# Optimization experiments

Hardware: AMD Instinct MI355X
Metric: run time of the kernel (lower is better)

## Reference

```python
import jax, jax.numpy as jnp
import numpy as np

B, SEQ = 64, 128
WV, PV = 50000, 50
WE, PE = 100, 25
HID = 400
DA, DR, NR = 500, 100, 46

_PARAMS = [
    ('word_emb', (WV, WE)), ('pos_emb', (PV, PE)),
    ('wi0f', (4*HID, WE+PE)), ('wh0f', (4*HID, HID)), ('b0f', (4*HID,)),
    ('wi0b', (4*HID, WE+PE)), ('wh0b', (4*HID, HID)), ('b0b', (4*HID,)),
    ('wi1f', (4*HID, 2*HID)), ('wh1f', (4*HID, HID)), ('b1f', (4*HID,)),
    ('wi1b', (4*HID, 2*HID)), ('wh1b', (4*HID, HID)), ('b1b', (4*HID,)),
    ('wi2f', (4*HID, 2*HID)), ('wh2f', (4*HID, HID)), ('b2f', (4*HID,)),
    ('wi2b', (4*HID, 2*HID)), ('wh2b', (4*HID, HID)), ('b2b', (4*HID,)),
    ('Wad', (2*HID, DA)), ('bad', (DA,)), ('Wah', (2*HID, DA)), ('bah', (DA,)),
    ('Wrd', (2*HID, DR)), ('brd', (DR,)), ('Wrh', (2*HID, DR)), ('brh', (DR,)),
    ('W_arc', (DA, DA)), ('b_arc', (DA,)),
    ('U_rel', (DR, NR, DR)), ('W_rel', (DR, NR)), ('b_rel', (NR,)),
]


def _run_dir(x, wi, wh, b, reverse):
    # x: (B, T, in). PyTorch LSTM gate order: i, f, g, o.
    pre = jnp.swapaxes(x, 0, 1) @ wi.T + b  # (T, B, 4H) input projection hoisted out of scan
    h0 = jnp.zeros((x.shape[0], wh.shape[1]), x.dtype)

    def step(carry, p):
        hp, cp = carry
        z = p + hp @ wh.T
        i, f, g, o = jnp.split(z, 4, axis=-1)
        c = jax.nn.sigmoid(f) * cp + jax.nn.sigmoid(i) * jnp.tanh(g)
        hn = jax.nn.sigmoid(o) * jnp.tanh(c)
        return (hn, c), hn

    _, ys = jax.lax.scan(step, (h0, h0), pre, reverse=reverse)
    return jnp.swapaxes(ys, 0, 1)  # (B, T, H)


def _bilstm(x, fwd, bwd):
    return jnp.concatenate([_run_dir(x, *fwd, reverse=False),
                            _run_dir(x, *bwd, reverse=True)], axis=-1)


def _forward(p, words, pos):
    # Embedding lookup + concat (dropout = identity in eval math)
    x = jnp.concatenate([p['word_emb'][words], p['pos_emb'][pos]], axis=-1)  # (B,SEQ,125)
    h = _bilstm(x, (p['wi0f'], p['wh0f'], p['b0f']), (p['wi0b'], p['wh0b'], p['b0b']))
    h = _bilstm(h, (p['wi1f'], p['wh1f'], p['b1f']), (p['wi1b'], p['wh1b'], p['b1b']))
    h = _bilstm(h, (p['wi2f'], p['wh2f'], p['b2f']), (p['wi2b'], p['wh2b'], p['b2b']))  # (B,SEQ,800)
    H_ah = jax.nn.relu(h @ p['Wah'] + p['bah'])
    H_ad = jax.nn.relu(h @ p['Wad'] + p['bad'])
    H_rh = jax.nn.relu(h @ p['Wrh'] + p['brh'])
    H_rd = jax.nn.relu(h @ p['Wrd'] + p['brd'])
    # Biaffine arc scores: S[b,i,j] = H_ad[b,i] W_arc H_ah[b,j] + b_arc . H_ah[b,j]
    S = jnp.einsum('bid,de,bje->bij', H_ad, p['W_arc'], H_ah) + (H_ah @ p['b_arc'])[:, None, :]
    head_preds = jnp.argmax(S, axis=2)  # (B, SEQ)
    # Original double python loop builds one_hot and bmm's it; that is exactly a row gather:
    H_rh_sel = jnp.take_along_axis(H_rh, head_preds[..., None], axis=1)  # (B,SEQ,DR)
    inter = jnp.einsum('bid,drk,bik->bir', H_rh_sel, p['U_rel'], H_rd)   # (B,SEQ,NR)
    sums = (H_rh_sel + H_rd) @ p['W_rel'] + p['b_rel']
    return S, inter + sums, head_preds


def setup_inputs() -> dict:
    key = jax.random.key(0)
    ks = jax.random.split(key, len(_PARAMS) + 2)
    out = {name: jax.random.normal(k, shape, jnp.float32) * 0.1
           for k, (name, shape) in zip(ks[:-2], _PARAMS)}
    out['words'] = jax.random.randint(ks[-2], (B, SEQ), 0, WV)
    out['pos'] = jax.random.randint(ks[-1], (B, SEQ), 0, PV)
    return out


def reference(words, pos, word_emb, pos_emb, wi0f, wh0f, b0f, wi0b, wh0b, b0b,
              wi1f, wh1f, b1f, wi1b, wh1b, b1b, wi2f, wh2f, b2f, wi2b, wh2b, b2b,
              Wad, bad, Wah, bah, Wrd, brd, Wrh, brh, W_arc, b_arc, U_rel, W_rel, b_rel):
    names = [n for n, _ in _PARAMS]
    vals = [word_emb, pos_emb, wi0f, wh0f, b0f, wi0b, wh0b, b0b,
            wi1f, wh1f, b1f, wi1b, wh1b, b1b, wi2f, wh2f, b2f, wi2b, wh2b, b2b,
            Wad, bad, Wah, bah, Wrd, brd, Wrh, brh, W_arc, b_arc, U_rel, W_rel, b_rel]
    return _forward(dict(zip(names, vals)), words, pos)
```

## Files before the change

### kernel.cpp

```cpp
#include <hip/hip_runtime.h>


#define TT 128
#define HID 400
#define G4 1600
#define NTOK 8192
#define NWD 100
#define CH 16

__global__ void embed_k(const int* __restrict__ words, const int* __restrict__ pos,
                        const float* __restrict__ wemb, const float* __restrict__ pemb,
                        float* __restrict__ x0) {
    int m = blockIdx.x;
    int t = m >> 6, b = m & 63;
    int tid = threadIdx.x;
    if (tid < 100) {
        x0[(size_t)m * 125 + tid] = wemb[(size_t)words[b * TT + t] * 100 + tid];
    } else if (tid < 125) {
        x0[(size_t)m * 125 + tid] = pemb[(size_t)pos[b * TT + t] * 25 + (tid - 100)];
    }
}

template <bool L0>
__global__ __launch_bounds__(256) void pre_k(
    const float* __restrict__ x0, const double* __restrict__ hF, const double* __restrict__ hB,
    const float* __restrict__ wiF, const float* __restrict__ wiB,
    const float* __restrict__ bF, const float* __restrict__ bB,
    double* __restrict__ prF, double* __restrict__ prB, int m0F, int m0B) {
    const int dir = blockIdx.z;
    const float* wi = dir ? wiB : wiF;
    const float* bias = dir ? bB : bF;
    double* pr = dir ? prB : prF;
    const int m0 = dir ? m0B : m0F;
    const int KP = L0 ? 128 : 800;

    __shared__ double As[16][66];
    __shared__ double Bs[16][66];

    const int tid = threadIdx.x;
    const int tm = tid >> 4, tn = tid & 15;
    const int bn = blockIdx.x * 64;
    const int y = blockIdx.y;
    const int tt = (m0 >> 6) + y;
    const int lane = tid & 63, kq = tid >> 6;

    double acc[4][4];
#pragma unroll
    for (int i = 0; i < 4; i++)
#pragma unroll
        for (int j = 0; j < 4; j++) acc[i][j] = 0.0;

    for (int k0 = 0; k0 < KP; k0 += 16) {
        if (L0) {
#pragma unroll
            for (int u = 0; u < 4; u++) {
                int k = k0 + kq * 4 + u;
                As[kq * 4 + u][lane] = (k < 125) ? (double)wi[(size_t)(bn + lane) * 125 + k] : 0.0;
            }
        } else {
            const float4 wv = *(const float4*)&wi[(size_t)(bn + lane) * 800 + k0 + kq * 4];
            As[kq * 4 + 0][lane] = (double)wv.x;
            As[kq * 4 + 1][lane] = (double)wv.y;
            As[kq * 4 + 2][lane] = (double)wv.z;
            As[kq * 4 + 3][lane] = (double)wv.w;
        }
        if (L0) {
#pragma unroll
            for (int u = 0; u < 4; u++) {
                int k = k0 + kq * 4 + u;
                Bs[kq * 4 + u][lane] = (k < 125) ? (double)x0[((size_t)tt * 64 + lane) * 125 + k] : 0.0;
            }
        } else {
            int kbase = k0 + kq * 4;
            const double* src = (kbase < 400) ? hF : hB;
            int kb = (kbase < 400) ? kbase : kbase - 400;
            const double* p = src + (size_t)tt * 25600 + (size_t)kb * 64 + lane;
#pragma unroll
            for (int u = 0; u < 4; u++) Bs[kq * 4 + u][lane] = p[(size_t)u * 64];
        }
        __syncthreads();
#pragma unroll
        for (int kk = 0; kk < 16; kk++) {
            double a[4], b[4];
#pragma unroll
            for (int i = 0; i < 4; i++) a[i] = As[kk][tm * 4 + i];
#pragma unroll
            for (int j = 0; j < 4; j++) b[j] = Bs[kk][tn * 4 + j];
#pragma unroll
            for (int i = 0; i < 4; i++)
#pragma unroll
                for (int j = 0; j < 4; j++) acc[i][j] = fma(a[i], b[j], acc[i][j]);
        }
        __syncthreads();
    }
#pragma unroll
    for (int i = 0; i < 4; i++) {
        int n = bn + tm * 4 + i;
        double bv = (double)bias[n];
#pragma unroll
        for (int j = 0; j < 4; j++)
            pr[((size_t)y * G4 + n) * 64 + (tn * 4 + j)] = acc[i][j] + bv;
    }
}

template <bool SPLITA, bool RELU, typename TC>
__global__ __launch_bounds__(256) void heads_k(
    const double* __restrict__ A, const double* __restrict__ AF, const double* __restrict__ AB,
    const float* __restrict__ Bm, const float* __restrict__ bias, TC* __restrict__ C,
    int N, int K, int ldb, int ldc, int OM) {
    __shared__ double As[16][66];
    __shared__ double Bs[16][66];
    const int tid = threadIdx.x;
    const int tm = tid >> 4, tn = tid & 15;
    const int bn = blockIdx.x * 64;
    const int bm = blockIdx.y * 64;
    const int lane = tid & 63, kq = tid >> 6;

    double acc[4][4];
#pragma unroll
    for (int i = 0; i < 4; i++)
#pragma unroll
        for (int j = 0; j < 4; j++) acc[i][j] = 0.0;

    const int KP = (K + 15) & ~15;
    for (int k0 = 0; k0 < KP; k0 += 16) {
        if (SPLITA) {
            int kbase = k0 + kq * 4;
            const double* src = (kbase < 400) ? AF : AB;
            int kb = (kbase < 400) ? kbase : kbase - 400;
            const double* p = src + (size_t)(bm >> 6) * 25600 + (size_t)kb * 64 + lane;
#pragma unroll
            for (int u = 0; u < 4; u++) As[kq * 4 + u][lane] = p[(size_t)u * 64];
        } else {
#pragma unroll
            for (int u = 0; u < 4; u++) {
                int k = k0 + kq * 4 + u;
                As[kq * 4 + u][lane] = (k < K) ? A[(size_t)(bm + lane) * K + k] : 0.0;
            }
        }
        {
            bool nok = (bn + lane) < N;
#pragma unroll
            for (int u = 0; u < 4; u++) {
                int k = k0 + kq * 4 + u;
                Bs[kq * 4 + u][lane] = (nok && k < K) ? (double)Bm[(size_t)k * ldb + bn + lane] : 0.0;
            }
        }
        __syncthreads();
#pragma unroll
        for (int kk = 0; kk < 16; kk++) {
            double a[4], b[4];
#pragma unroll
            for (int i = 0; i < 4; i++) a[i] = As[kk][tm * 4 + i];
#pragma unroll
            for (int j = 0; j < 4; j++) b[j] = Bs[kk][tn * 4 + j];
#pragma unroll
            for (int i = 0; i < 4; i++)
#pragma unroll
                for (int j = 0; j < 4; j++) acc[i][j] = fma(a[i], b[j], acc[i][j]);
        }
        __syncthreads();
    }
#pragma unroll
    for (int i = 0; i < 4; i++) {
        int row = bm + tm * 4 + i;
        size_t orow = (OM == 0) ? (size_t)row
                                : ((size_t)(row & 63) * TT + (row >> 6));
#pragma unroll
        for (int j = 0; j < 4; j++) {
            int n = bn + tn * 4 + j;
            if (n >= N) continue;
            double v = acc[i][j] + (bias ? (double)bias[n] : 0.0);
            if (RELU) v = fmax(v, 0.0);
            C[orow * ldc + n] = (TC)v;
        }
    }
}

__global__ __launch_bounds__(512) void lstm_k(
    const double* __restrict__ preF, const double* __restrict__ preB,
    const float* __restrict__ whF, const float* __restrict__ whB,
    double* __restrict__ hsF, double* __restrict__ hsB,
    double* __restrict__ csF, double* __restrict__ csB,
    int* __restrict__ flagsF, int* __restrict__ flagsB, int ci) {
    const int wg = blockIdx.x;
    const int dir = wg / NWD;
    const int wgd = wg % NWD;
    const double* pre = dir ? preB : preF;
    const float* wh = dir ? whB : whF;
    double* hs = dir ? hsB : hsF;
    double* cs = dir ? csB : csF;
    int* flags = dir ? flagsB : flagsF;
    const int tid = threadIdx.x;
    const int b = tid & 63;
    const int w = tid >> 6;
    const int tlb = dir ? (TT - CH - ci * CH) : ci * CH;

    __shared__ double whl[4][HID][4];
    __shared__ double pl[8][4][4][64];
    for (int idx = tid; idx < 4 * HID * 4; idx += 512) {
        int g = idx & 3; int k = (idx >> 2) % HID; int jx = idx / (4 * HID);
        whl[jx][k][g] = (double)wh[((size_t)g * HID + wgd * 4 + jx) * HID + k];
    }
    __syncthreads();

    const int jown = wgd * 4 + (w & 3);
    double c = 0.0;
    if (w < 4) c = (ci == 0) ? 0.0 : cs[(size_t)jown * 64 + b];

    for (int s = 0; s < CH; ++s) {
        const int sg = ci * CH + s;
        const int t = dir ? (TT - 1 - sg) : sg;
        double z0[4];
        if (w < 4) {
            const double* pp = pre + (size_t)(t - tlb) * (G4 * 64) + b;
#pragma unroll
            for (int g = 0; g < 4; g++) z0[g] = pp[(size_t)(g * HID + jown) * 64];
        }
        if (sg > 0) {
            if (w == 0) {
                bool need2 = b < (NWD - 64);
                for (;;) {
                    int f1 = __hip_atomic_load(&flags[b], __ATOMIC_RELAXED, __HIP_MEMORY_SCOPE_AGENT);
                    int f2 = need2 ? __hip_atomic_load(&flags[64 + b], __ATOMIC_RELAXED, __HIP_MEMORY_SCOPE_AGENT)
                                   : 0x7fffffff;
                    if (__all(f1 >= sg && f2 >= sg)) break;
                    __builtin_amdgcn_s_sleep(1);
                }
                __builtin_amdgcn_fence(__ATOMIC_ACQUIRE, "agent");
            }
            __syncthreads();
        }
        double part[4][4];
#pragma unroll
        for (int j = 0; j < 4; j++)
#pragma unroll
            for (int g = 0; g < 4; g++) part[j][g] = 0.0;
        if (sg > 0) {
            const int tp = dir ? (t + 1) : (t - 1);
            const double* hp = hs + (size_t)tp * (HID * 64) + b;
#pragma unroll 5
            for (int k = w * 50; k < w * 50 + 50; ++k) {
                double hv = hp[(size_t)k * 64];
#pragma unroll
                for (int j = 0; j < 4; j++)
#pragma unroll
                    for (int g = 0; g < 4; g++)
                        part[j][g] = fma(hv, whl[j][k][g], part[j][g]);
            }
        }
#pragma unroll
        for (int j = 0; j < 4; j++)
#pragma unroll
            for (int g = 0; g < 4; g++) pl[w][j][g][b] = part[j][g];
        __syncthreads();
        if (w < 4) {
            double z[4];
#pragma unroll
            for (int g = 0; g < 4; g++) {
                double acc = z0[g];
#pragma unroll
                for (int q = 0; q < 8; q++) acc += pl[q][w][g][b];
                z[g] = acc;
            }
            double si = 1.0 / (1.0 + exp(-z[0]));
            double sf = 1.0 / (1.0 + exp(-z[1]));
            double tg = tanh(z[2]);
            double so = 1.0 / (1.0 + exp(-z[3]));
            c = sf * c + si * tg;
            double h = so * tanh(c);
            __hip_atomic_store(&hs[(size_t)t * (HID * 64) + (size_t)jown * 64 + b], h,
                               __ATOMIC_RELAXED, __HIP_MEMORY_SCOPE_AGENT);
        }
        __syncthreads();
        if (tid == 0)
            __hip_atomic_store(&flags[wgd], sg + 1, __ATOMIC_RELEASE, __HIP_MEMORY_SCOPE_AGENT);
    }
    if (w < 4) cs[(size_t)jown * 64 + b] = c;
}

__global__ void bh_k(const double* __restrict__ Hah, const float* __restrict__ barc,
                     double* __restrict__ bh) {
    int row = blockIdx.x * 4 + (threadIdx.x >> 6);
    int lane = threadIdx.x & 63;
    const double* r = Hah + (size_t)row * 500;
    double s = 0.0;
    for (int e = lane; e < 500; e += 64) s = fma(r[e], (double)barc[e], s);
    for (int off = 32; off; off >>= 1) s += __shfl_down(s, off, 64);
    if (lane == 0) bh[row] = s;
}

__global__ __launch_bounds__(256) void s_k(const double* __restrict__ HadW,
                                           const double* __restrict__ Hah,
                                           const double* __restrict__ bh,
                                           double* __restrict__ S64,
                                           float* __restrict__ Sf) {
    int b = blockIdx.z;
    int i = blockIdx.y * 16 + threadIdx.y;
    int j = blockIdx.x * 16 + threadIdx.x;
    const double* ra = HadW + ((size_t)b * TT + i) * 500;
    const double* rb = Hah + ((size_t)b * TT + j) * 500;
    double s = 0.0;
#pragma unroll 4
    for (int e = 0; e < 500; ++e) s = fma(ra[e], rb[e], s);
    double v = s + bh[b * TT + j];
    size_t o = ((size_t)b * TT + i) * TT + j;
    S64[o] = v;
    Sf[o] = (float)v;
}

__global__ void argmax_k(const double* __restrict__ S64, int* __restrict__ headi,
                         float* __restrict__ headf) {
    int row = blockIdx.x * 4 + (threadIdx.x >> 6);
    int lane = threadIdx.x & 63;
    const double* r = S64 + (size_t)row * TT;
    double v0 = r[lane], v1 = r[lane + 64];
    double m = fmax(v0, v1);
    for (int off = 32; off; off >>= 1) m = fmax(m, __shfl_down(m, off, 64));
    m = __shfl(m, 0, 64);
    double tau = 1e-4 + 3e-6 * fabs(m);
    int c = 999;
    if (v1 >= m - tau) c = lane + 64;
    if (v0 >= m - tau) c = lane;
    for (int off = 32; off; off >>= 1) {
        int oc = __shfl_down(c, off, 64);
        c = min(c, oc);
    }
    if (lane == 0) { headi[row] = c; headf[row] = (float)c; }
}

__global__ __launch_bounds__(320) void rel_k(
    const float* __restrict__ Hrh, const float* __restrict__ Hrd,
    const int* __restrict__ headi, const float* __restrict__ U,
    const float* __restrict__ Wrel, const float* __restrict__ brel,
    float* __restrict__ out) {
    __shared__ float sel[32][105];
    __shared__ float rd[32][105];
    __shared__ float red[32][12];
    int tid = threadIdx.x;
    int blk = blockIdx.x;
    for (int idx = tid; idx < 32 * 100; idx += 320) {
        int tt2 = idx / 100, d = idx % 100;
        int tok = blk * 32 + tt2;
        int b = tok >> 7;
        int hp = headi[tok] & 127;
        sel[tt2][d] = Hrh[((size_t)(b << 7) + hp) * 100 + d];
        rd[tt2][d] = Hrd[(size_t)tok * 100 + d];
    }
    __syncthreads();
    int tt2 = tid & 31;
    int dg = tid >> 5;
    int tok = blk * 32 + tt2;
    int r0 = blockIdx.y * 6;
    int r1 = min(46, r0 + 6);
    for (int r = r0; r < r1; ++r) {
        float acc = 0.f;
#pragma unroll
        for (int dd = 0; dd < 10; dd += 2) {
            int d = dg * 10 + dd;
            const float4* uA = (const float4*)(U + ((size_t)d * 46 + r) * 100);
            const float4* uB = (const float4*)(U + ((size_t)(d + 1) * 46 + r) * 100);
            float a0 = 0.f, a1 = 0.f, a2 = 0.f, a3 = 0.f;
            float b0 = 0.f, b1 = 0.f, b2 = 0.f, b3 = 0.f;
#pragma unroll
            for (int q = 0; q < 25; ++q) {
                float4 ua = uA[q], ub = uB[q];
                float r0v = rd[tt2][4 * q + 0], r1v = rd[tt2][4 * q + 1];
                float r2v = rd[tt2][4 * q + 2], r3v = rd[tt2][4 * q + 3];
                a0 = fmaf(ua.x, r0v, a0); a1 = fmaf(ua.y, r1v, a1);
                a2 = fmaf(ua.z, r2v, a2); a3 = fmaf(ua.w, r3v, a3);
                b0 = fmaf(ub.x, r0v, b0); b1 = fmaf(ub.y, r1v, b1);
                b2 = fmaf(ub.z, r2v, b2); b3 = fmaf(ub.w, r3v, b3);
            }
            acc = fmaf(sel[tt2][d], (a0 + a1) + (a2 + a3), acc);
            acc = fmaf(sel[tt2][d + 1], (b0 + b1) + (b2 + b3), acc);
        }
        if (dg == 0) {
            float sdot = 0.f;
#pragma unroll 4
            for (int k = 0; k < 100; ++k)
                sdot = fmaf(sel[tt2][k] + rd[tt2][k], Wrel[k * 46 + r], sdot);
            acc += sdot + brel[r];
        }
        red[tt2][dg] = acc;
        __syncthreads();
        if (dg == 0) {
            float tot = 0.f;
#pragma unroll
            for (int q = 0; q < 10; ++q) tot += red[tt2][q];
            out[(size_t)tok * 46 + r] = tot;
        }
        __syncthreads();
    }
}

extern "C" void kernel_launch(void* const* d_in, const int* in_sizes, int n_in,
                              void* d_out, int out_size, void* d_ws, size_t ws_size,
                              hipStream_t stream) {
    const float* wemb = (const float*)d_in[0];
    const float* pemb = (const float*)d_in[1];
    const float* wi[3][2] = {{(const float*)d_in[2], (const float*)d_in[5]},
                             {(const float*)d_in[8], (const float*)d_in[11]},
                             {(const float*)d_in[14], (const float*)d_in[17]}};
    const float* wh[3][2] = {{(const float*)d_in[3], (const float*)d_in[6]},
                             {(const float*)d_in[9], (const float*)d_in[12]},
                             {(const float*)d_in[15], (const float*)d_in[18]}};
    const float* bia[3][2] = {{(const float*)d_in[4], (const float*)d_in[7]},
                              {(const float*)d_in[10], (const float*)d_in[13]},
                              {(const float*)d_in[16], (const float*)d_in[19]}};
    const float* Wad = (const float*)d_in[20]; const float* bad = (const float*)d_in[21];
    const float* Wah = (const float*)d_in[22]; const float* bah = (const float*)d_in[23];
    const float* Wrd = (const float*)d_in[24]; const float* brd = (const float*)d_in[25];
    const float* Wrh = (const float*)d_in[26]; const float* brh = (const float*)d_in[27];
    const float* Warc = (const float*)d_in[28]; const float* barc = (const float*)d_in[29];
    const float* U = (const float*)d_in[30];
    const float* Wrel = (const float*)d_in[31]; const float* brel = (const float*)d_in[32];
    const int* words = (const int*)d_in[33];
    const int* pos = (const int*)d_in[34];

    char* ws = (char*)d_ws;
    double* hsA  = (double*)(ws + 0);
    double* hsB  = (double*)(ws + 52428800);
    float*  x0   = (float*)(ws + 52428800);
    double* preF = (double*)(ws + 104857600);
    double* preB = (double*)(ws + 117964800);
    double* Hah64  = (double*)(ws + 52428800);
    double* Had64  = (double*)(ws + 85196800);
    float*  Hrh    = (float*)(ws + 117964800);
    float*  Hrd    = (float*)(ws + 121241600);
    double* S64    = (double*)(ws + 124518400);
    double* bh64   = (double*)(ws + 132907008);
    int*    headi  = (int*)(ws + 132972544);
    double* HadW64 = (double*)(ws + 0);
    double* csF  = (double*)d_out;
    double* csB  = (double*)((char*)d_out + 204800);
    int*    flags = (int*)((char*)d_out + 409600);

    float* Sf = (float*)d_out;
    float* rel = Sf + 1048576;
    float* headf = Sf + 1425408;

    hipMemsetAsync(flags, 0, 768 * sizeof(int), stream);
    embed_k<<<NTOK, 128, 0, stream>>>(words, pos, wemb, pemb, x0);

    const size_t HALF = 3276800;
    dim3 gPre(25, CH, 2);
    for (int l = 0; l < 3; ++l) {
        double* ho = (l == 1) ? hsB : hsA;
        const double* hiF = (l == 0) ? nullptr : ((l == 1) ? hsA : hsB);
        const double* hiB = hiF ? hiF + HALF : nullptr;
        for (int ci = 0; ci < 8; ++ci) {
            int m0F = ci * CH * 64;
            int m0B = (TT - CH - ci * CH) * 64;
            if (l == 0)
                pre_k<true><<<gPre, 256, 0, stream>>>(x0, nullptr, nullptr,
                    wi[0][0], wi[0][1], bia[0][0], bia[0][1], preF, preB, m0F, m0B);
            else
                pre_k<false><<<gPre, 256, 0, stream>>>(nullptr, hiF, hiB,
                    wi[l][0], wi[l][1], bia[l][0], bia[l][1], preF, preB, m0F, m0B);
            lstm_k<<<2 * NWD, 512, 0, stream>>>(preF, preB, wh[l][0], wh[l][1],
                ho, ho + HALF, csF, csB,
                flags + (l * 2 + 0) * 128, flags + (l * 2 + 1) * 128, ci);
        }
    }
    const double* fF = hsA; const double* fB = hsA + HALF;
    heads_k<true, true, double><<<dim3(8, 128), 256, 0, stream>>>(
        nullptr, fF, fB, Wah, bah, Hah64, 500, 800, 500, 500, 1);
    heads_k<true, true, double><<<dim3(8, 128), 256, 0, stream>>>(
        nullptr, fF, fB, Wad, bad, Had64, 500, 800, 500, 500, 0);
    heads_k<true, true, float><<<dim3(2, 128), 256, 0, stream>>>(
        nullptr, fF, fB, Wrh, brh, Hrh, 100, 800, 100, 100, 1);
    heads_k<true, true, float><<<dim3(2, 128), 256, 0, stream>>>(
        nullptr, fF, fB, Wrd, brd, Hrd, 100, 800, 100, 100, 1);
    heads_k<false, false, double><<<dim3(8, 128), 256, 0, stream>>>(
        Had64, nullptr, nullptr, Warc, nullptr, HadW64, 500, 500, 500, 500, 1);

    bh_k<<<NTOK / 4, 256, 0, stream>>>(Hah64, barc, bh64);
    s_k<<<dim3(8, 8, 64), dim3(16, 16), 0, stream>>>(HadW64, Hah64, bh64, S64, Sf);
    argmax_k<<<NTOK / 4, 256, 0, stream>>>(S64, headi, headf);
    rel_k<<<dim3(NTOK / 32, 8), 320, 0, stream>>>(Hrh, Hrd, headi, U, Wrel, brel, rel);
}
```

Baseline: 10.63 ms.

## Fuse LSTM recurrence with next-chunk input projection in one double-buffered kernel

Merges the per-chunk input-projection GEMM and the LSTM recurrence into a single kernel. The first 200 blocks run the recurrence for chunk ci while the remaining blocks compute the projection for chunk ci+1 into a second, double-buffered pre-activation buffer. Chunk size is halved to 8 steps and there are 16 chunks per layer. The LSTM block also shrinks from 512 threads with a cross-wave partial-sum reduction to 256 threads, each wave owning one hidden unit and doing the full k loop. The GEMM thread-to-element mapping is changed to a strided layout, and the S dot product gets four independent accumulators. This hides projection time behind the serial recurrence, at the cost of more kernel launches and longer per-thread recurrence loops.

```diff
diff --git a/kernel.cpp b/kernel.cpp
--- a/kernel.cpp
+++ b/kernel.cpp
@@ -6,7 +6,8 @@
 #define G4 1600
 #define NTOK 8192
 #define NWD 100
-#define CH 16
+#define CH 8
+#define NCH 16
 
 __global__ void embed_k(const int* __restrict__ words, const int* __restrict__ pos,
                         const float* __restrict__ wemb, const float* __restrict__ pemb,
@@ -22,84 +23,158 @@
 }
 
 template <bool L0>
-__global__ __launch_bounds__(256) void pre_k(
+__global__ __launch_bounds__(256) void fused_k(
     const float* __restrict__ x0, const double* __restrict__ hF, const double* __restrict__ hB,
     const float* __restrict__ wiF, const float* __restrict__ wiB,
     const float* __restrict__ bF, const float* __restrict__ bB,
-    double* __restrict__ prF, double* __restrict__ prB, int m0F, int m0B) {
-    const int dir = blockIdx.z;
-    const float* wi = dir ? wiB : wiF;
-    const float* bias = dir ? bB : bF;
-    double* pr = dir ? prB : prF;
-    const int m0 = dir ? m0B : m0F;
-    const int KP = L0 ? 128 : 800;
-
-    __shared__ double As[16][66];
-    __shared__ double Bs[16][66];
-
+    double* __restrict__ preW, const double* __restrict__ preR,
+    const float* __restrict__ whF, const float* __restrict__ whB,
+    double* __restrict__ hsF, double* __restrict__ hsB,
+    double* __restrict__ csF, double* __restrict__ csB,
+    int* __restrict__ flagsF, int* __restrict__ flagsB,
+    int ci, int nLstm) {
+    __shared__ __align__(16) char smraw[51200];
     const int tid = threadIdx.x;
-    const int tm = tid >> 4, tn = tid & 15;
-    const int bn = blockIdx.x * 64;
-    const int y = blockIdx.y;
-    const int tt = (m0 >> 6) + y;
-    const int lane = tid & 63, kq = tid >> 6;
-
-    double acc[4][4];
-#pragma unroll
-    for (int i = 0; i < 4; i++)
-#pragma unroll
-        for (int j = 0; j < 4; j++) acc[i][j] = 0.0;
-
-    for (int k0 = 0; k0 < KP; k0 += 16) {
-        if (L0) {
-#pragma unroll
-            for (int u = 0; u < 4; u++) {
-                int k = k0 + kq * 4 + u;
-                As[kq * 4 + u][lane] = (k < 125) ? (double)wi[(size_t)(bn + lane) * 125 + k] : 0.0;
-            }
-        } else {
-            const float4 wv = *(const float4*)&wi[(size_t)(bn + lane) * 800 + k0 + kq * 4];
-            As[kq * 4 + 0][lane] = (double)wv.x;
-            As[kq * 4 + 1][lane] = (double)wv.y;
-            As[kq * 4 + 2][lane] = (double)wv.z;
-            As[kq * 4 + 3][lane] = (double)wv.w;
-        }
-        if (L0) {
-#pragma unroll
-            for (int u = 0; u < 4; u++) {
-                int k = k0 + kq * 4 + u;
-                Bs[kq * 4 + u][lane] = (k < 125) ? (double)x0[((size_t)tt * 64 + lane) * 125 + k] : 0.0;
-            }
-        } else {
-            int kbase = k0 + kq * 4;
-            const double* src = (kbase < 400) ? hF : hB;
-            int kb = (kbase < 400) ? kbase : kbase - 400;
-            const double* p = src + (size_t)tt * 25600 + (size_t)kb * 64 + lane;
-#pragma unroll
-            for (int u = 0; u < 4; u++) Bs[kq * 4 + u][lane] = p[(size_t)u * 64];
+
+    if ((int)blockIdx.x < nLstm) {
+        double (*whl)[HID][4] = (double(*)[HID][4])smraw;
+        const int wg = blockIdx.x;
+        const int dir = wg / NWD;
+        const int wgd = wg % NWD;
+        const double* pre = preR + (size_t)dir * 819200;
+        const float* wh = dir ? whB : whF;
+        double* hs = dir ? hsB : hsF;
+        double* cs = dir ? csB : csF;
+        int* flags = dir ? flagsB : flagsF;
+        const int b = tid & 63;
+        const int w = tid >> 6;
+        const int tlb = dir ? (TT - CH - ci * CH) : ci * CH;
+
+        for (int idx = tid; idx < 4 * HID * 4; idx += 256) {
+            int g = idx & 3; int k = (idx >> 2) % HID; int jx = idx / (4 * HID);
+            whl[jx][k][g] = (double)wh[((size_t)g * HID + wgd * 4 + jx) * HID + k];
         }
         __syncthreads();
-#pragma unroll
-        for (int kk = 0; kk < 16; kk++) {
-            double a[4], b[4];
-#pragma unroll
-            for (int i = 0; i < 4; i++) a[i] = As[kk][tm * 4 + i];
-#pragma unroll
-            for (int j = 0; j < 4; j++) b[j] = Bs[kk][tn * 4 + j];
-#pragma unroll
-            for (int i = 0; i < 4; i++)
-#pragma unroll
-                for (int j = 0; j < 4; j++) acc[i][j] = fma(a[i], b[j], acc[i][j]);
-        }
-        __syncthreads();
-    }
-#pragma unroll
-    for (int i = 0; i < 4; i++) {
-        int n = bn + tm * 4 + i;
-        double bv = (double)bias[n];
-#pragma unroll
-        for (int j = 0; j < 4; j++)
-            pr[((size_t)y * G4 + n) * 64 + (tn * 4 + j)] = acc[i][j] + bv;
+
+        const int jown = wgd * 4 + w;
+        double c = (ci == 0) ? 0.0 : cs[(size_t)jown * 64 + b];
+
+        for (int s = 0; s < CH; ++s) {
+            const int sg = ci * CH + s;
+            const int t = dir ? (TT - 1 - sg) : sg;
+            double z[4];
+            {
+                const double* pp = pre + (size_t)(t - tlb) * (G4 * 64) + b;
+#pragma unroll
+                for (int g = 0; g < 4; g++) z[g] = pp[(size_t)(g * HID + jown) * 64];
+            }
+            if (sg > 0) {
+                if (w == 0) {
+                    bool need2 = b < (NWD - 64);
+                    for (;;) {
+                        int f1 = __hip_atomic_load(&flags[b], __ATOMIC_RELAXED, __HIP_MEMORY_SCOPE_AGENT);
+                        int f2 = need2 ? __hip_atomic_load(&flags[64 + b], __ATOMIC_RELAXED, __HIP_MEMORY_SCOPE_AGENT)
+                                       : 0x7fffffff;
+                        if (__all(f1 >= sg && f2 >= sg)) break;
+                        __builtin_amdgcn_s_sleep(1);
+                    }
+                    __builtin_amdgcn_fence(__ATOMIC_ACQUIRE, "agent");
+                }
+                __syncthreads();
+                const int tp = dir ? (t + 1) : (t - 1);
+                const double* hp = hs + (size_t)tp * (HID * 64) + b;
+#pragma unroll 4
+                for (int k = 0; k < HID; ++k) {
+                    double hv = hp[(size_t)k * 64];
+                    const double* w4 = &whl[w][k][0];
+                    z[0] = fma(hv, w4[0], z[0]);
+                    z[1] = fma(hv, w4[1], z[1]);
+                    z[2] = fma(hv, w4[2], z[2]);
+                    z[3] = fma(hv, w4[3], z[3]);
+                }
+            }
+            double si = 1.0 / (1.0 + exp(-z[0]));
+            double sf = 1.0 / (1.0 + exp(-z[1]));
+            double tg = tanh(z[2]);
+            double so = 1.0 / (1.0 + exp(-z[3]));
+            c = sf * c + si * tg;
+            double h = so * tanh(c);
+            __hip_atomic_store(&hs[(size_t)t * (HID * 64) + (size_t)jown * 64 + b], h,
+                               __ATOMIC_RELAXED, __HIP_MEMORY_SCOPE_AGENT);
+            __syncthreads();
+            if (tid == 0)
+                __hip_atomic_store(&flags[wgd], sg + 1, __ATOMIC_RELEASE, __HIP_MEMORY_SCOPE_AGENT);
+        }
+        cs[(size_t)jown * 64 + b] = c;
+    } else {
+        const int cn = ci + 1;
+        if (cn >= NCH) return;
+        double (*As)[66] = (double(*)[66])smraw;
+        double (*Bs)[66] = (double(*)[66])(smraw + 8448);
+        int tile = blockIdx.x - nLstm;
+        int nt = tile % 25;
+        int rest = tile / 25;
+        int y = rest & 7;
+        int dirp = rest >> 3;
+        const float* wi = dirp ? wiB : wiF;
+        const float* bias = dirp ? bB : bF;
+        double* pr = preW + (size_t)dirp * 819200;
+        const int tt = dirp ? (TT - CH - cn * CH) + y : cn * CH + y;
+        const int bn = nt * 64;
+        const int tm = tid >> 4, tn = tid & 15;
+        const int lane = tid & 63, kq = tid >> 6;
+
+        double acc[4][4];
+#pragma unroll
+        for (int i = 0; i < 4; i++)
+#pragma unroll
+            for (int j = 0; j < 4; j++) acc[i][j] = 0.0;
+
+        const int KP = L0 ? 128 : 800;
+        for (int k0 = 0; k0 < KP; k0 += 16) {
+            if (L0) {
+#pragma unroll
+                for (int u = 0; u < 4; u++) {
+                    int k = k0 + kq * 4 + u;
+                    As[kq * 4 + u][lane] = (k < 125) ? (double)wi[(size_t)(bn + lane) * 125 + k] : 0.0;
+                    Bs[kq * 4 + u][lane] = (k < 125) ? (double)x0[((size_t)tt * 64 + lane) * 125 + k] : 0.0;
+                }
+            } else {
+                const float4 wv = *(const float4*)&wi[(size_t)(bn + lane) * 800 + k0 + kq * 4];
+                As[kq * 4 + 0][lane] = (double)wv.x;
+                As[kq * 4 + 1][lane] = (double)wv.y;
+                As[kq * 4 + 2][lane] = (double)wv.z;
+                As[kq * 4 + 3][lane] = (double)wv.w;
+                int kbase = k0 + kq * 4;
+                const double* src = (kbase < 400) ? hF : hB;
+                int kb = (kbase < 400) ? kbase : kbase - 400;
+                const double* p = src + (size_t)tt * 25600 + (size_t)kb * 64 + lane;
+#pragma unroll
+                for (int u = 0; u < 4; u++) Bs[kq * 4 + u][lane] = p[(size_t)u * 64];
+            }
+            __syncthreads();
+#pragma unroll
+            for (int kk = 0; kk < 16; kk++) {
+                double a[4], bv[4];
+#pragma unroll
+                for (int i = 0; i < 4; i++) a[i] = As[kk][i * 16 + tm];
+#pragma unroll
+                for (int j = 0; j < 4; j++) bv[j] = Bs[kk][j * 16 + tn];
+#pragma unroll
+                for (int i = 0; i < 4; i++)
+#pragma unroll
+                    for (int j = 0; j < 4; j++) acc[i][j] = fma(a[i], bv[j], acc[i][j]);
+            }
+            __syncthreads();
+        }
+#pragma unroll
+        for (int i = 0; i < 4; i++) {
+            int n = bn + i * 16 + tm;
+            double bv = (double)bias[n];
+#pragma unroll
+            for (int j = 0; j < 4; j++)
+                pr[((size_t)y * G4 + n) * 64 + (j * 16 + tn)] = acc[i][j] + bv;
+        }
     }
 }
 
@@ -149,134 +224,32 @@
         __syncthreads();
 #pragma unroll
         for (int kk = 0; kk < 16; kk++) {
-            double a[4], b[4];
-#pragma unroll
-            for (int i = 0; i < 4; i++) a[i] = As[kk][tm * 4 + i];
-#pragma unroll
-            for (int j = 0; j < 4; j++) b[j] = Bs[kk][tn * 4 + j];
+            double a[4], bv[4];
+#pragma unroll
+            for (int i = 0; i < 4; i++) a[i] = As[kk][i * 16 + tm];
+#pragma unroll
+            for (int j = 0; j < 4; j++) bv[j] = Bs[kk][j * 16 + tn];
 #pragma unroll
             for (int i = 0; i < 4; i++)
 #pragma unroll
-                for (int j = 0; j < 4; j++) acc[i][j] = fma(a[i], b[j], acc[i][j]);
+                for (int j = 0; j < 4; j++) acc[i][j] = fma(a[i], bv[j], acc[i][j]);
         }
         __syncthreads();
     }
 #pragma unroll
     for (int i = 0; i < 4; i++) {
-        int row = bm + tm * 4 + i;
+        int row = bm + i * 16 + tm;
         size_t orow = (OM == 0) ? (size_t)row
                                 : ((size_t)(row & 63) * TT + (row >> 6));
 #pragma unroll
         for (int j = 0; j < 4; j++) {
-            int n = bn + tn * 4 + j;
+            int n = bn + j * 16 + tn;
             if (n >= N) continue;
             double v = acc[i][j] + (bias ? (double)bias[n] : 0.0);
             if (RELU) v = fmax(v, 0.0);
             C[orow * ldc + n] = (TC)v;
         }
     }
-}
-
-__global__ __launch_bounds__(512) void lstm_k(
-    const double* __restrict__ preF, const double* __restrict__ preB,
-    const float* __restrict__ whF, const float* __restrict__ whB,
-    double* __restrict__ hsF, double* __restrict__ hsB,
-    double* __restrict__ csF, double* __restrict__ csB,
-    int* __restrict__ flagsF, int* __restrict__ flagsB, int ci) {
-    const int wg = blockIdx.x;
-    const int dir = wg / NWD;
-    const int wgd = wg % NWD;
-    const double* pre = dir ? preB : preF;
-    const float* wh = dir ? whB : whF;
-    double* hs = dir ? hsB : hsF;
-    double* cs = dir ? csB : csF;
-    int* flags = dir ? flagsB : flagsF;
-    const int tid = threadIdx.x;
-    const int b = tid & 63;
-    const int w = tid >> 6;
-    const int tlb = dir ? (TT - CH - ci * CH) : ci * CH;
-
-    __shared__ double whl[4][HID][4];
-    __shared__ double pl[8][4][4][64];
-    for (int idx = tid; idx < 4 * HID * 4; idx += 512) {
-        int g = idx & 3; int k = (idx >> 2) % HID; int jx = idx / (4 * HID);
-        whl[jx][k][g] = (double)wh[((size_t)g * HID + wgd * 4 + jx) * HID + k];
-    }
-    __syncthreads();
-
-    const int jown = wgd * 4 + (w & 3);
-    double c = 0.0;
-    if (w < 4) c = (ci == 0) ? 0.0 : cs[(size_t)jown * 64 + b];
-
-    for (int s = 0; s < CH; ++s) {
-        const int sg = ci * CH + s;
-        const int t = dir ? (TT - 1 - sg) : sg;
-        double z0[4];
-        if (w < 4) {
-            const double* pp = pre + (size_t)(t - tlb) * (G4 * 64) + b;
-#pragma unroll
-            for (int g = 0; g < 4; g++) z0[g] = pp[(size_t)(g * HID + jown) * 64];
-        }
-        if (sg > 0) {
-            if (w == 0) {
-                bool need2 = b < (NWD - 64);
-                for (;;) {
-                    int f1 = __hip_atomic_load(&flags[b], __ATOMIC_RELAXED, __HIP_MEMORY_SCOPE_AGENT);
-                    int f2 = need2 ? __hip_atomic_load(&flags[64 + b], __ATOMIC_RELAXED, __HIP_MEMORY_SCOPE_AGENT)
-                                   : 0x7fffffff;
-                    if (__all(f1 >= sg && f2 >= sg)) break;
-                    __builtin_amdgcn_s_sleep(1);
-                }
-                __builtin_amdgcn_fence(__ATOMIC_ACQUIRE, "agent");
-            }
-            __syncthreads();
-        }
-        double part[4][4];
-#pragma unroll
-        for (int j = 0; j < 4; j++)
-#pragma unroll
-            for (int g = 0; g < 4; g++) part[j][g] = 0.0;
-        if (sg > 0) {
-            const int tp = dir ? (t + 1) : (t - 1);
-            const double* hp = hs + (size_t)tp * (HID * 64) + b;
-#pragma unroll 5
-            for (int k = w * 50; k < w * 50 + 50; ++k) {
-                double hv = hp[(size_t)k * 64];
-#pragma unroll
-                for (int j = 0; j < 4; j++)
-#pragma unroll
-                    for (int g = 0; g < 4; g++)
-                        part[j][g] = fma(hv, whl[j][k][g], part[j][g]);
-            }
-        }
-#pragma unroll
-        for (int j = 0; j < 4; j++)
-#pragma unroll
-            for (int g = 0; g < 4; g++) pl[w][j][g][b] = part[j][g];
-        __syncthreads();
-        if (w < 4) {
-            double z[4];
-#pragma unroll
-            for (int g = 0; g < 4; g++) {
-                double acc = z0[g];
-#pragma unroll
-                for (int q = 0; q < 8; q++) acc += pl[q][w][g][b];
-                z[g] = acc;
-            }
-            double si = 1.0 / (1.0 + exp(-z[0]));
-            double sf = 1.0 / (1.0 + exp(-z[1]));
-            double tg = tanh(z[2]);
-            double so = 1.0 / (1.0 + exp(-z[3]));
-            c = sf * c + si * tg;
-            double h = so * tanh(c);
-            __hip_atomic_store(&hs[(size_t)t * (HID * 64) + (size_t)jown * 64 + b], h,
-                               __ATOMIC_RELAXED, __HIP_MEMORY_SCOPE_AGENT);
-        }
-        __syncthreads();
-        if (tid == 0)
-            __hip_atomic_store(&flags[wgd], sg + 1, __ATOMIC_RELEASE, __HIP_MEMORY_SCOPE_AGENT);
-    }
-    if (w < 4) cs[(size_t)jown * 64 + b] = c;
 }
 
 __global__ void bh_k(const double* __restrict__ Hah, const float* __restrict__ barc,
@@ -300,10 +273,15 @@
     int j = blockIdx.x * 16 + threadIdx.x;
     const double* ra = HadW + ((size_t)b * TT + i) * 500;
     const double* rb = Hah + ((size_t)b * TT + j) * 500;
-    double s = 0.0;
+    double s0 = 0.0, s1 = 0.0, s2 = 0.0, s3 = 0.0;
 #pragma unroll 4
-    for (int e = 0; e < 500; ++e) s = fma(ra[e], rb[e], s);
-    double v = s + bh[b * TT + j];
+    for (int e = 0; e < 500; e += 4) {
+        s0 = fma(ra[e + 0], rb[e + 0], s0);
+        s1 = fma(ra[e + 1], rb[e + 1], s1);
+        s2 = fma(ra[e + 2], rb[e + 2], s2);
+        s3 = fma(ra[e + 3], rb[e + 3], s3);
+    }
+    double v = ((s0 + s1) + (s2 + s3)) + bh[b * TT + j];
     size_t o = ((size_t)b * TT + i) * TT + j;
     S64[o] = v;
     Sf[o] = (float)v;
@@ -422,8 +400,7 @@
     double* hsA  = (double*)(ws + 0);
     double* hsB  = (double*)(ws + 52428800);
     float*  x0   = (float*)(ws + 52428800);
-    double* preF = (double*)(ws + 104857600);
-    double* preB = (double*)(ws + 117964800);
+    double* preBase = (double*)(ws + 104857600);
     double* Hah64  = (double*)(ws + 52428800);
     double* Had64  = (double*)(ws + 85196800);
     float*  Hrh    = (float*)(ws + 117964800);
@@ -444,34 +421,47 @@
     embed_k<<<NTOK, 128, 0, stream>>>(words, pos, wemb, pemb, x0);
 
     const size_t HALF = 3276800;
-    dim3 gPre(25, CH, 2);
+    const size_t PREBUF = 1638400;
     for (int l = 0; l < 3; ++l) {
         double* ho = (l == 1) ? hsB : hsA;
         const double* hiF = (l == 0) ? nullptr : ((l == 1) ? hsA : hsB);
         const double* hiB = hiF ? hiF + HALF : nullptr;
-        for (int ci = 0; ci < 8; ++ci) {
-            int m0F = ci * CH * 64;
-            int m0B = (TT - CH - ci * CH) * 64;
+        int* fF = flags + (l * 2 + 0) * 128;
+        int* fB = flags + (l * 2 + 1) * 128;
+        if (l == 0)
+            fused_k<true><<<400, 256, 0, stream>>>(x0, nullptr, nullptr,
+                wi[0][0], wi[0][1], bia[0][0], bia[0][1],
+                preBase, preBase + PREBUF, wh[0][0], wh[0][1],
+                ho, ho + HALF, csF, csB, fF, fB, -1, 0);
+        else
+            fused_k<false><<<400, 256, 0, stream>>>(nullptr, hiF, hiB,
+                wi[l][0], wi[l][1], bia[l][0], bia[l][1],
+                preBase, preBase + PREBUF, wh[l][0], wh[l][1],
+                ho, ho + HALF, csF, csB, fF, fB, -1, 0);
+        for (int ci = 0; ci < NCH; ++ci) {
+            double* preR = preBase + (size_t)(ci & 1) * PREBUF;
+            double* preW = preBase + (size_t)((ci + 1) & 1) * PREBUF;
             if (l == 0)
-                pre_k<true><<<gPre, 256, 0, stream>>>(x0, nullptr, nullptr,
-                    wi[0][0], wi[0][1], bia[0][0], bia[0][1], preF, preB, m0F, m0B);
+                fused_k<true><<<600, 256, 0, stream>>>(x0, nullptr, nullptr,
+                    wi[0][0], wi[0][1], bia[0][0], bia[0][1],
+                    preW, preR, wh[0][0], wh[0][1],
+                    ho, ho + HALF, csF, csB, fF, fB, ci, 2 * NWD);
             else
-                pre_k<false><<<gPre, 256, 0, stream>>>(nullptr, hiF, hiB,
-                    wi[l][0], wi[l][1], bia[l][0], bia[l][1], preF, preB, m0F, m0B);
-            lstm_k<<<2 * NWD, 512, 0, stream>>>(preF, preB, wh[l][0], wh[l][1],
-                ho, ho + HALF, csF, csB,
-                flags + (l * 2 + 0) * 128, flags + (l * 2 + 1) * 128, ci);
-        }
-    }
-    const double* fF = hsA; const double* fB = hsA + HALF;
+                fused_k<false><<<600, 256, 0, stream>>>(nullptr, hiF, hiB,
+                    wi[l][0], wi[l][1], bia[l][0], bia[l][1],
+                    preW, preR, wh[l][0], wh[l][1],
+                    ho, ho + HALF, csF, csB, fF, fB, ci, 2 * NWD);
+        }
+    }
+    const double* fF2 = hsA; const double* fB2 = hsA + HALF;
     heads_k<true, true, double><<<dim3(8, 128), 256, 0, stream>>>(
-        nullptr, fF, fB, Wah, bah, Hah64, 500, 800, 500, 500, 1);
+        nullptr, fF2, fB2, Wah, bah, Hah64, 500, 800, 500, 500, 1);
     heads_k<true, true, double><<<dim3(8, 128), 256, 0, stream>>>(
-        nullptr, fF, fB, Wad, bad, Had64, 500, 800, 500, 500, 0);
+        nullptr, fF2, fB2, Wad, bad, Had64, 500, 800, 500, 500, 0);
     heads_k<true, true, float><<<dim3(2, 128), 256, 0, stream>>>(
-        nullptr, fF, fB, Wrh, brh, Hrh, 100, 800, 100, 100, 1);
+        nullptr, fF2, fB2, Wrh, brh, Hrh, 100, 800, 100, 100, 1);
     heads_k<true, true, float><<<dim3(2, 128), 256, 0, stream>>>(
-        nullptr, fF, fB, Wrd, brd, Hrd, 100, 800, 100, 100, 1);
+        nullptr, fF2, fB2, Wrd, brd, Hrd, 100, 800, 100, 100, 1);
     heads_k<false, false, double><<<dim3(8, 128), 256, 0, stream>>>(
         Had64, nullptr, nullptr, Warc, nullptr, HadW64, 500, 500, 500, 500, 1);
 
```

After: 16.06 ms. 1.51x slower.
